# Optimization experiments

Hardware: AMD Instinct MI355X
Metric: run time of the kernel (lower is better)

The kernel has to match this reference:

```python
import jax, jax.numpy as jnp
import numpy as np

B, S, D, H, NUM_REL = 8, 1024, 1024, 16, 512
HD = D // H  # head size = 64


def setup_inputs() -> dict:
    key = jax.random.key(0)
    ks = jax.random.split(key, 12)
    sc = 0.02  # weight init scale for numerical stability
    inp = {
        "query": jax.random.normal(ks[0], (B, S, D), jnp.float32),
        "key": jax.random.normal(ks[1], (B, S, D), jnp.float32),
        "value": jax.random.normal(ks[2], (B, S, D), jnp.float32),
        "Wq": jax.random.normal(ks[3], (D, D), jnp.float32) * sc,
        "bq": jnp.zeros((D,), jnp.float32),
        "Wk": jax.random.normal(ks[4], (D, D), jnp.float32) * sc,
        "bk": jnp.zeros((D,), jnp.float32),
        "Wv": jax.random.normal(ks[5], (D, D), jnp.float32) * sc,
        "bv": jnp.zeros((D,), jnp.float32),
        "Wo": jax.random.normal(ks[6], (D, D), jnp.float32) * sc,
        "bo": jnp.zeros((D,), jnp.float32),
        "pos_table": jax.random.normal(ks[7], (NUM_REL, HD), jnp.float32) * sc,
        # True = masked position (causal: cannot attend to future)
        "mask": jnp.broadcast_to(jnp.triu(jnp.ones((S, S), bool), k=1), (B, S, S)),
    }
    return inp


def reference(query, key, value, Wq, bq, Wk, bk, Wv, bv, Wo, bo, pos_table, mask):
    Bq, Sq, Dm = query.shape
    hd = Dm // H

    def proj(x, W, b):
        # nn.Linear: x @ W.T + b, then split heads -> [B, H, S, hd]
        return (x @ W.T + b).reshape(Bq, Sq, H, hd).transpose(0, 2, 1, 3)

    q = proj(query, Wq, bq)
    k = proj(key, Wk, bk)
    v = proj(value, Wv, bv)

    scores = jnp.einsum("bhid,bhjd->bhij", q, k)

    # relative-position bias: idxs[i,j] = clip(i - j, 0, NUM_REL-1)
    t = jnp.arange(Sq)
    idxs = jnp.clip(t[:, None] - t[None, :], 0, pos_table.shape[0] - 1)
    pos = pos_table[idxs]  # [S, S, hd]
    scores = scores + jnp.einsum("bhid,ijd->bhij", q, pos)

    scores = scores / np.sqrt(hd).astype(np.float32)
    scores = jnp.where(mask[:, None, :, :], jnp.float32(-1e9), scores)
    prob = jax.nn.softmax(scores, axis=-1)  # dropout p=0.0 -> identity

    out = jnp.einsum("bhij,bhjd->bhid", prob, v)
    out = out.transpose(0, 2, 1, 3).reshape(Bq, Sq, Dm)
    return out @ Wo.T + bo
```

## Files before the change

### kernel.cpp

```cpp
#include <hip/hip_runtime.h>
#include <stdint.h>

#define DEV __device__ __forceinline__

typedef unsigned short u16;
typedef __bf16 bf16x8 __attribute__((ext_vector_type(8)));
typedef float  f32x4  __attribute__((ext_vector_type(4)));
typedef unsigned short u16x8 __attribute__((ext_vector_type(8)));
typedef unsigned short u16x4 __attribute__((ext_vector_type(4)));
typedef float  fvec4  __attribute__((ext_vector_type(4)));

constexpr int Sz   = 1024;
constexpr int Dm   = 1024;
constexpr int HDm  = 64;
constexpr int NREL = 512;
constexpr int Mrows = 8192;
constexpr int KV   = 32;

DEV u16 f2bf(float f) { return __builtin_bit_cast(u16, (__bf16)f); }
DEV float bf2f(u16 h) { return __builtin_bit_cast(float, (uint32_t)h << 16); }
DEV f32x4 mfma16(bf16x8 a, bf16x8 b, f32x4 c) {
  return __builtin_amdgcn_mfma_f32_16x16x32_bf16(a, b, c, 0, 0, 0);
}
DEV float ex2(float x) {
  float r;
  asm("v_exp_f32 %0, %1" : "=v"(r) : "v"(x));
  return r;
}

DEV u16x4 tr0(const u16* p) {
  u16x4 d;
  asm volatile("ds_read_b64_tr_b16 %0, %1"
               : "=v"(d)
               : "v"((const __attribute__((address_space(3))) u16*)p));
  return d;
}
DEV u16x4 tr512(const u16* p) {
  u16x4 d;
  asm volatile("ds_read_b64_tr_b16 %0, %1 offset:512"
               : "=v"(d)
               : "v"((const __attribute__((address_space(3))) u16*)p));
  return d;
}
DEV bf16x8 mk8(u16x4 a, u16x4 b) {
  u16x8 r;
  r[0] = a[0]; r[1] = a[1]; r[2] = a[2]; r[3] = a[3];
  r[4] = b[0]; r[5] = b[1]; r[6] = b[2]; r[7] = b[3];
  return __builtin_bit_cast(bf16x8, r);
}
DEV void gload(const u16* src, u16* dst) {
  __builtin_amdgcn_global_load_lds(
      (const __attribute__((address_space(1))) void*)src,
      (__attribute__((address_space(3))) void*)dst, 16, 0, 0);
}

__global__ __launch_bounds__(256) void cvtw_kernel(const float* __restrict__ w0,
                                                   const float* __restrict__ w1,
                                                   const float* __restrict__ w2,
                                                   const float* __restrict__ w3,
                                                   const float* __restrict__ ps,
                                                   u16* __restrict__ o0,
                                                   u16* __restrict__ o1,
                                                   u16* __restrict__ o2,
                                                   u16* __restrict__ o3,
                                                   u16* __restrict__ op) {
  const int bid = blockIdx.x;
  const float* in;
  u16* out;
  int local;
  if (bid < 4096) {
    const int s = bid >> 10;
    in = s == 0 ? w0 : s == 1 ? w1 : s == 2 ? w2 : w3;
    out = s == 0 ? o0 : s == 1 ? o1 : s == 2 ? o2 : o3;
    local = bid & 1023;
  } else {
    in = ps; out = op; local = bid - 4096;
  }
  size_t i = (size_t)local * 256 + threadIdx.x;
  fvec4 v = *(const fvec4*)(in + i * 4);
  u16x4 o;
  o[0] = f2bf(v[0]); o[1] = f2bf(v[1]); o[2] = f2bf(v[2]); o[3] = f2bf(v[3]);
  *(u16x4*)(out + i * 4) = o;
}

template<bool OUT_BF16>
DEV void gemm_epilogue(const float* bias, void* Cout, int m0, int n0,
                       int wr, int wc, int lr, int lg, f32x4 acc[4][4]) {
  #pragma unroll
  for (int m = 0; m < 4; ++m) {
    const int grow = m0 + wr + m * 16 + lr;
    #pragma unroll
    for (int n = 0; n < 4; ++n) {
      const int gcol = n0 + wc + n * 16 + lg * 4;
      fvec4 bb = *(const fvec4*)&bias[gcol];
      if (OUT_BF16) {
        u16x4 w;
        #pragma unroll
        for (int r = 0; r < 4; ++r) w[r] = f2bf(acc[m][n][r] + bb[r]);
        *(u16x4*)&((u16*)Cout)[(size_t)grow * Dm + gcol] = w;
      } else {
        fvec4 w;
        #pragma unroll
        for (int r = 0; r < 4; ++r) w[r] = acc[m][n][r] + bb[r];
        *(fvec4*)&((float*)Cout)[(size_t)grow * Dm + gcol] = w;
      }
    }
  }
}

DEV void gemm_compute(const u16* Ab, const u16* Bb, int wr, int wc,
                      int lr, int lg, f32x4 acc[4][4]) {
  #pragma unroll
  for (int kk = 0; kk < 2; ++kk) {
    bf16x8 af[4], bf_[4];
    #pragma unroll
    for (int m = 0; m < 4; ++m)
      af[m] = *(const bf16x8*)&Ab[(wr + m * 16 + lr) * 64 + (((kk * 4 + lg) ^ (lr & 7)) * 8)];
    #pragma unroll
    for (int n = 0; n < 4; ++n)
      bf_[n] = *(const bf16x8*)&Bb[(wc + n * 16 + lr) * 64 + (((kk * 4 + lg) ^ (lr & 7)) * 8)];
    __builtin_amdgcn_s_setprio(1);
    #pragma unroll
    for (int m = 0; m < 4; ++m)
      #pragma unroll
      for (int n = 0; n < 4; ++n)
        acc[m][n] = mfma16(bf_[n], af[m], acc[m][n]);
    __builtin_amdgcn_s_setprio(0);
  }
}

template<bool OUT_BF16>
DEV void gemm_body16(const u16* __restrict__ A, const u16* __restrict__ Bw,
                     const float* __restrict__ bias, void* __restrict__ Cout,
                     int m0, int n0, u16* As, u16* Bs) {
  const int tid = threadIdx.x;
  const int wave = tid >> 6, lane = tid & 63;
  const int lr = lane & 15, lg = lane >> 4;
  const int wr = (wave >> 1) * 64, wc = (wave & 1) * 64;

  auto issue = [&](int t) {
    const int k0 = t * 64;
    u16* Ad = As + (t & 1) * (128 * 64);
    u16* Bd = Bs + (t & 1) * (128 * 64);
    #pragma unroll
    for (int it = 0; it < 4; ++it) {
      int chunk = it * 256 + tid;
      int row = chunk >> 3, c16 = chunk & 7;
      gload(Bw + (size_t)(n0 + row) * Dm + k0 + ((c16 ^ (row & 7)) * 8),
            Bd + (it * 256 + wave * 64) * 8);
      gload(A + (size_t)(m0 + row) * Dm + k0 + ((c16 ^ (row & 7)) * 8),
            Ad + (it * 256 + wave * 64) * 8);
    }
  };

  issue(0);
  f32x4 acc[4][4] = {};
  for (int t = 0; t < 16; ++t) {
    if (t < 15) {
      issue(t + 1);
      asm volatile("s_waitcnt vmcnt(8)" ::: "memory");
    } else {
      asm volatile("s_waitcnt vmcnt(0)" ::: "memory");
    }
    __builtin_amdgcn_s_barrier();
    gemm_compute(As + (t & 1) * (128 * 64), Bs + (t & 1) * (128 * 64),
                 wr, wc, lr, lg, acc);
    __builtin_amdgcn_s_barrier();
  }
  gemm_epilogue<OUT_BF16>(bias, Cout, m0, n0, wr, wc, lr, lg, acc);
}

template<bool OUT_BF16>
DEV void gemm_body32(const float* __restrict__ A, const u16* __restrict__ Bw,
                     const float* __restrict__ bias, void* __restrict__ Cout,
                     int m0, int n0, u16* As, u16* Bs) {
  const int tid = threadIdx.x;
  const int wave = tid >> 6, lane = tid & 63;
  const int lr = lane & 15, lg = lane >> 4;
  const int wr = (wave >> 1) * 64, wc = (wave & 1) * 64;
  const int row = tid >> 3 << 2, c16 = tid & 7;

  auto issueB = [&](int t) {
    const int k0 = t * 64;
    u16* Bd = Bs + (t & 1) * (128 * 64);
    #pragma unroll
    for (int it = 0; it < 4; ++it) {
      int chunk = it * 256 + tid;
      int rw = chunk >> 3, cc = chunk & 7;
      gload(Bw + (size_t)(n0 + rw) * Dm + k0 + ((cc ^ (rw & 7)) * 8),
            Bd + (it * 256 + wave * 64) * 8);
    }
  };

  fvec4 ar[4][2];
  auto loadA = [&](int t) {
    const int k0 = t * 64;
    #pragma unroll
    for (int it = 0; it < 4; ++it) {
      int chunk = it * 256 + tid;
      int rw = chunk >> 3, cc = chunk & 7;
      const float* src = A + (size_t)(m0 + rw) * Dm + k0 + cc * 8;
      ar[it][0] = *(const fvec4*)src;
      ar[it][1] = *(const fvec4*)(src + 4);
    }
  };

  issueB(0);
  loadA(0);
  f32x4 acc[4][4] = {};
  for (int t = 0; t < 16; ++t) {
    asm volatile("s_waitcnt vmcnt(0)" ::: "memory");
    u16* Ad = As + (t & 1) * (128 * 64);
    #pragma unroll
    for (int it = 0; it < 4; ++it) {
      int chunk = it * 256 + tid;
      int rw = chunk >> 3, cc = chunk & 7;
      u16x8 v;
      #pragma unroll
      for (int e = 0; e < 4; ++e) { v[e] = f2bf(ar[it][0][e]); v[e + 4] = f2bf(ar[it][1][e]); }
      *(u16x8*)&Ad[rw * 64 + ((cc ^ (rw & 7)) * 8)] = v;
    }
    if (t < 15) { issueB(t + 1); loadA(t + 1); }
    asm volatile("s_waitcnt lgkmcnt(0)" ::: "memory");
    __builtin_amdgcn_s_barrier();
    gemm_compute(Ad, Bs + (t & 1) * (128 * 64), wr, wc, lr, lg, acc);
    __builtin_amdgcn_s_barrier();
  }
  gemm_epilogue<OUT_BF16>(bias, Cout, m0, n0, wr, wc, lr, lg, acc);
}

template<bool OUT_BF16>
__global__ __launch_bounds__(256) void gemm1_kernel(const u16* __restrict__ A,
                                                    const u16* __restrict__ Bw,
                                                    const float* __restrict__ bias,
                                                    void* __restrict__ Cout) {
  __shared__ u16 As[2 * 128 * 64];
  __shared__ u16 Bs[2 * 128 * 64];
  const int r = blockIdx.x;
  const int xcd = r & 7, loc = r >> 3;
  const int m0 = (xcd * 8 + (loc & 7)) * 128;
  const int n0 = (loc >> 3) * 128;
  gemm_body16<OUT_BF16>(A, Bw, bias, Cout, m0, n0, As, Bs);
}

__global__ __launch_bounds__(256) void gemm3_kernel(
    const float* __restrict__ Xq, const float* __restrict__ Xk, const float* __restrict__ Xv,
    const u16* __restrict__ Wq, const u16* __restrict__ Wk, const u16* __restrict__ Wv,
    const float* __restrict__ bq, const float* __restrict__ bk, const float* __restrict__ bv,
    u16* __restrict__ Cq, u16* __restrict__ Ck, u16* __restrict__ Cv) {
  __shared__ u16 As[2 * 128 * 64];
  __shared__ u16 Bs[2 * 128 * 64];
  const int flat = blockIdx.x;
  const int seg = flat >> 9;
  const int r = flat & 511;
  const int xcd = r & 7, loc = r >> 3;
  const int m0 = (xcd * 8 + (loc & 7)) * 128;
  const int n0 = (loc >> 3) * 128;
  const float* A = seg == 0 ? Xq : seg == 1 ? Xk : Xv;
  const u16* Bw = seg == 0 ? Wq : seg == 1 ? Wk : Wv;
  const float* bias = seg == 0 ? bq : seg == 1 ? bk : bv;
  u16* C = seg == 0 ? Cq : seg == 1 ? Ck : Cv;
  gemm_body32<true>(A, Bw, bias, C, m0, n0, As, Bs);
}

__global__ __launch_bounds__(256, 4) void attn_kernel(const u16* __restrict__ Q,
                                                      const u16* __restrict__ Kb,
                                                      const u16* __restrict__ Vb,
                                                      const u16* __restrict__ posB,
                                                      u16* __restrict__ O) {
  __shared__ u16 Ks[2][KV * 64];
  __shared__ u16 Vs[2][KV * 64];
  __shared__ u16 ring[128 * 64];
  __shared__ u16 SH[4][16 * 40];

  const int tid = threadIdx.x;
  const int wave = tid >> 6, lane = tid & 63;
  const int lr = lane & 15, lg = lane >> 4;
  const int bid = blockIdx.x;
  const int xcd = bid & 7;
  const int idx = bid >> 3;
  const int bhl = idx & 15;
  const int pp_ = idx >> 4;
  const int bh  = xcd * 16 + bhl;
  const int b = bh >> 4, h = bh & 15;

  u16* SHW = SH[wave];
  const size_t rowbase = (size_t)(b * Sz) * Dm + h * HDm;

  const int krow = tid >> 3, kc = tid & 7;
  const int vj = ((tid >> 5) << 2) | ((tid >> 1) & 3);
  const int vd = ((tid >> 3) & 3) * 16 + (tid & 1) * 8;
  const int rrow = tid >> 3, rcol = tid & 7;

  auto issueKV = [&](int t) {
    const int j0 = t * KV;
    const int bsel = t & 1;
    gload(Kb + rowbase + (size_t)(j0 + krow) * Dm + ((kc ^ (krow & 7)) * 8),
          &Ks[bsel][wave * 512]);
    gload(Vb + rowbase + (size_t)(j0 + vj) * Dm + vd, &Vs[bsel][wave * 512]);
  };
  auto stageRing = [&](int cb) {
    const int rel = cb + rrow;
    const int slot = rel & 127;
    const int cl = rel < 0 ? 0 : (rel > NREL - 1 ? NREL - 1 : rel);
    gload(posB + cl * 64 + ((rcol ^ (slot & 7)) * 8),
          &ring[((cb & 127) + wave * 8) * 64]);
  };

  constexpr float SC = 0.125f * 1.44269504f;

  for (int job = 0; job < 2; ++job) {
    const int qi = job ? pp_ : 15 - pp_;
    const int qb = qi * 64;
    const int wq = qb + wave * 16;
    const int nt = 2 * qi + 2;
    const int qg = wq + lr;

    const u16* qptr = Q + rowbase + (size_t)(wq + lr) * Dm;
    bf16x8 qf[2];
    qf[0] = *(const bf16x8*)(qptr + lg * 8);
    qf[1] = *(const bf16x8*)(qptr + 32 + lg * 8);

    float b511;
    {
      const u16* pp = posB + (NREL - 1) * HDm;
      bf16x8 pa0 = *(const bf16x8*)(pp + lg * 8);
      bf16x8 pa1 = *(const bf16x8*)(pp + 32 + lg * 8);
      f32x4 a = {};
      a = mfma16(pa0, qf[0], a);
      a = mfma16(pa1, qf[1], a);
      b511 = a[0];
    }

    stageRing(qb + 32);
    stageRing(qb);
    stageRing(qb - 32);
    issueKV(0);

    f32x4 oacc[4] = {};
    float m_i = -1e30f, l_i = 0.f;

    for (int t = 0; t < nt; ++t) {
      const int j0 = t * KV;
      const int bsel = t & 1;
      const bool active = (j0 <= wq + 15);
      const bool clamp = (wq - j0 - 31) >= NREL - 1;
      const int wb = wq - j0 - 31;

      if (t + 1 < nt) {
        stageRing(qb - 32 * (t + 1) - 32);
        issueKV(t + 1);
        asm volatile("s_waitcnt vmcnt(3)" ::: "memory");
      } else {
        asm volatile("s_waitcnt vmcnt(0)" ::: "memory");
      }
      __builtin_amdgcn_s_barrier();

      if (active) {
        if (!clamp) {
          #pragma unroll
          for (int wg = 0; wg < 3; ++wg) {
            const int rrel = wb + wg * 16 + lr;
            const int slot = rrel & 127;
            const u16* rp = &ring[slot * 64];
            f32x4 a = {};
            a = mfma16(qf[0], *(const bf16x8*)&rp[((0 + lg) ^ (slot & 7)) * 8], a);
            a = mfma16(qf[1], *(const bf16x8*)&rp[((4 + lg) ^ (slot & 7)) * 8], a);
            #pragma unroll
            for (int r = 0; r < 4; ++r) {
              const int q = lg * 4 + r;
              const int col = q - (wg * 16 + lr) + 31;
              if (col >= 0 && col < 32)
                SHW[q * 40 + col] = f2bf(a[r]);
            }
          }
        }

        __builtin_amdgcn_s_setprio(1);
        f32x4 s0 = {}, s1 = {};
        const u16* KT = &Ks[bsel][0];
        s0 = mfma16(*(const bf16x8*)&KT[(0 + lr) * 64 + (((0 + lg) ^ (lr & 7)) * 8)], qf[0], s0);
        s0 = mfma16(*(const bf16x8*)&KT[(0 + lr) * 64 + (((4 + lg) ^ (lr & 7)) * 8)], qf[1], s0);
        s1 = mfma16(*(const bf16x8*)&KT[(16 + lr) * 64 + (((0 + lg) ^ (lr & 7)) * 8)], qf[0], s1);
        s1 = mfma16(*(const bf16x8*)&KT[(16 + lr) * 64 + (((4 + lg) ^ (lr & 7)) * 8)], qf[1], s1);
        __builtin_amdgcn_s_setprio(0);

        float p0[4], p1[4];
        float tmax = -3e38f;
        if (clamp) {
          #pragma unroll
          for (int r = 0; r < 4; ++r) {
            p0[r] = (s0[r] + b511) * SC; tmax = fmaxf(tmax, p0[r]);
            p1[r] = (s1[r] + b511) * SC; tmax = fmaxf(tmax, p1[r]);
          }
        } else {
          u16x4 bv0 = *(const u16x4*)&SHW[lr * 40 + lg * 4];
          u16x4 bv1 = *(const u16x4*)&SHW[lr * 40 + 16 + lg * 4];
          #pragma unroll
          for (int r = 0; r < 4; ++r) {
            float v0 = (s0[r] + bf2f(bv0[r])) * SC;
            if (j0 + lg * 4 + r > qg) v0 = -1e9f;
            p0[r] = v0; tmax = fmaxf(tmax, v0);
            float v1 = (s1[r] + bf2f(bv1[r])) * SC;
            if (j0 + 16 + lg * 4 + r > qg) v1 = -1e9f;
            p1[r] = v1; tmax = fmaxf(tmax, v1);
          }
        }
        tmax = fmaxf(tmax, __shfl_xor(tmax, 16));
        tmax = fmaxf(tmax, __shfl_xor(tmax, 32));

        if (!__all(tmax <= m_i + 11.5f)) {
          float mn = fmaxf(m_i, tmax);
          float sc = ex2(m_i - mn);
          m_i = mn; l_i *= sc;
          #pragma unroll
          for (int dg = 0; dg < 4; ++dg) oacc[dg] *= sc;
        }

        float lsum = 0.f;
        #pragma unroll
        for (int r = 0; r < 4; ++r) {
          p0[r] = ex2(p0[r] - m_i); lsum += p0[r];
          p1[r] = ex2(p1[r] - m_i); lsum += p1[r];
        }
        lsum += __shfl_xor(lsum, 16);
        lsum += __shfl_xor(lsum, 32);
        l_i += lsum;

        u16x4 pk0, pk1;
        #pragma unroll
        for (int r = 0; r < 4; ++r) { pk0[r] = f2bf(p0[r]); pk1[r] = f2bf(p1[r]); }
        *(u16x4*)&SHW[lr * 40 + lg * 4] = pk0;
        *(u16x4*)&SHW[lr * 40 + 16 + lg * 4] = pk1;

        bf16x8 pB = *(const bf16x8*)&SHW[lr * 40 + lg * 8];

        u16x4 va[4][2];
        #pragma unroll
        for (int dg = 0; dg < 4; ++dg) {
          const u16* base = &Vs[bsel][(2 * lg) * 256 + dg * 64 + lr * 4];
          va[dg][0] = tr0(base);
          va[dg][1] = tr512(base);
        }
        asm volatile("s_waitcnt lgkmcnt(0)" ::: "memory");
        __builtin_amdgcn_sched_barrier(0);
        __builtin_amdgcn_s_setprio(1);
        #pragma unroll
        for (int dg = 0; dg < 4; ++dg)
          oacc[dg] = mfma16(mk8(va[dg][0], va[dg][1]), pB, oacc[dg]);
        __builtin_amdgcn_s_setprio(0);
      }
      __builtin_amdgcn_s_barrier();
    }

    const float inv = 1.0f / l_i;
    const size_t obase = rowbase + (size_t)qg * Dm;
    #pragma unroll
    for (int dg = 0; dg < 4; ++dg) {
      u16x4 w;
      #pragma unroll
      for (int r = 0; r < 4; ++r) w[r] = f2bf(oacc[dg][r] * inv);
      *(u16x4*)&O[obase + dg * 16 + lg * 4] = w;
    }
  }
}

extern "C" void kernel_launch(void* const* d_in, const int* in_sizes, int n_in,
                              void* d_out, int out_size, void* d_ws, size_t ws_size,
                              hipStream_t stream) {
  const float* query = (const float*)d_in[0];
  const float* key   = (const float*)d_in[1];
  const float* value = (const float*)d_in[2];
  const float* Wq    = (const float*)d_in[3];
  const float* bq    = (const float*)d_in[4];
  const float* Wk    = (const float*)d_in[5];
  const float* bk    = (const float*)d_in[6];
  const float* Wv    = (const float*)d_in[7];
  const float* bv    = (const float*)d_in[8];
  const float* Wo    = (const float*)d_in[9];
  const float* bo    = (const float*)d_in[10];
  const float* pos   = (const float*)d_in[11];

  char* ws = (char*)d_ws;
  u16* WqB  = (u16*)(ws);
  u16* WkB  = (u16*)(ws + (2ull << 20));
  u16* WvB  = (u16*)(ws + (4ull << 20));
  u16* WoB  = (u16*)(ws + (6ull << 20));
  u16* posB = (u16*)(ws + (8ull << 20));
  u16* Qb   = (u16*)(ws + (9ull << 20));
  u16* Kb   = (u16*)(ws + (25ull << 20));
  u16* Vb   = (u16*)(ws + (41ull << 20));
  u16* Ob   = (u16*)(ws + (57ull << 20));

  cvtw_kernel<<<4128, 256, 0, stream>>>(Wq, Wk, Wv, Wo, pos,
                                        WqB, WkB, WvB, WoB, posB);

  gemm3_kernel<<<1536, 256, 0, stream>>>(query, key, value, WqB, WkB, WvB,
                                         bq, bk, bv, Qb, Kb, Vb);

  attn_kernel<<<1024, 256, 0, stream>>>(Qb, Kb, Vb, posB, Ob);

  gemm1_kernel<false><<<512, 256, 0, stream>>>(Ob, WoB, bo, d_out);
}
```

Baseline: 185.0 us.

## Shrink GEMM K-tile to 32 with triple-buffered LDS and deeper prefetch

Both projection GEMM bodies move from a 64-wide K tile with double buffering to a 32-wide K tile with three rotating LDS buffers and a prefetch distance of two tiles. The A operand in the fp32 GEMM is held in two alternating register sets and written into a single bf16 LDS tile. The swizzle changes to fit 32-element rows, and launch bounds now request 4 blocks per CU. This cuts LDS use per block to raise occupancy and hide global-load latency, at the cost of twice as many barriers per K and more register pressure.

```diff
diff --git a/kernel.cpp b/kernel.cpp
--- a/kernel.cpp
+++ b/kernel.cpp
@@ -108,25 +108,28 @@
   }
 }
 
-DEV void gemm_compute(const u16* Ab, const u16* Bb, int wr, int wc,
-                      int lr, int lg, f32x4 acc[4][4]) {
+DEV void gemm_compute32(const u16* Ab, const u16* Bb, int wr, int wc,
+                        int lr, int lg, f32x4 (&acc)[4][4]) {
+  bf16x8 af[4], bf_[4];
   #pragma unroll
-  for (int kk = 0; kk < 2; ++kk) {
-    bf16x8 af[4], bf_[4];
-    #pragma unroll
-    for (int m = 0; m < 4; ++m)
-      af[m] = *(const bf16x8*)&Ab[(wr + m * 16 + lr) * 64 + (((kk * 4 + lg) ^ (lr & 7)) * 8)];
+  for (int m = 0; m < 4; ++m) {
+    const int row = wr + m * 16 + lr;
+    const int s = ((row >> 2) ^ row) & 3;
+    af[m] = *(const bf16x8*)&Ab[row * 32 + ((lg ^ s) * 8)];
+  }
+  #pragma unroll
+  for (int n = 0; n < 4; ++n) {
+    const int row = wc + n * 16 + lr;
+    const int s = ((row >> 2) ^ row) & 3;
+    bf_[n] = *(const bf16x8*)&Bb[row * 32 + ((lg ^ s) * 8)];
+  }
+  __builtin_amdgcn_s_setprio(1);
+  #pragma unroll
+  for (int m = 0; m < 4; ++m)
     #pragma unroll
     for (int n = 0; n < 4; ++n)
-      bf_[n] = *(const bf16x8*)&Bb[(wc + n * 16 + lr) * 64 + (((kk * 4 + lg) ^ (lr & 7)) * 8)];
-    __builtin_amdgcn_s_setprio(1);
-    #pragma unroll
-    for (int m = 0; m < 4; ++m)
-      #pragma unroll
-      for (int n = 0; n < 4; ++n)
-        acc[m][n] = mfma16(bf_[n], af[m], acc[m][n]);
-    __builtin_amdgcn_s_setprio(0);
-  }
+      acc[m][n] = mfma16(bf_[n], af[m], acc[m][n]);
+  __builtin_amdgcn_s_setprio(0);
 }
 
 template<bool OUT_BF16>
@@ -139,32 +142,34 @@
   const int wr = (wave >> 1) * 64, wc = (wave & 1) * 64;
 
   auto issue = [&](int t) {
-    const int k0 = t * 64;
-    u16* Ad = As + (t & 1) * (128 * 64);
-    u16* Bd = Bs + (t & 1) * (128 * 64);
+    const int k0 = t * 32;
+    u16* Ad = As + (t % 3) * (128 * 32);
+    u16* Bd = Bs + (t % 3) * (128 * 32);
     #pragma unroll
-    for (int it = 0; it < 4; ++it) {
-      int chunk = it * 256 + tid;
-      int row = chunk >> 3, c16 = chunk & 7;
-      gload(Bw + (size_t)(n0 + row) * Dm + k0 + ((c16 ^ (row & 7)) * 8),
-            Bd + (it * 256 + wave * 64) * 8);
-      gload(A + (size_t)(m0 + row) * Dm + k0 + ((c16 ^ (row & 7)) * 8),
-            Ad + (it * 256 + wave * 64) * 8);
+    for (int c = 0; c < 2; ++c) {
+      const int chunk = c * 256 + tid;
+      const int row = chunk >> 2, g = chunk & 3;
+      const int s = ((row >> 2) ^ row) & 3;
+      gload(A + (size_t)(m0 + row) * Dm + k0 + ((g ^ s) * 8),
+            Ad + c * 2048 + wave * 512);
+      gload(Bw + (size_t)(n0 + row) * Dm + k0 + ((g ^ s) * 8),
+            Bd + c * 2048 + wave * 512);
     }
   };
 
   issue(0);
+  issue(1);
   f32x4 acc[4][4] = {};
-  for (int t = 0; t < 16; ++t) {
-    if (t < 15) {
-      issue(t + 1);
-      asm volatile("s_waitcnt vmcnt(8)" ::: "memory");
+  for (int t = 0; t < 32; ++t) {
+    if (t < 31) {
+      asm volatile("s_waitcnt vmcnt(4)" ::: "memory");
     } else {
       asm volatile("s_waitcnt vmcnt(0)" ::: "memory");
     }
+    if (t < 30) issue(t + 2);
     __builtin_amdgcn_s_barrier();
-    gemm_compute(As + (t & 1) * (128 * 64), Bs + (t & 1) * (128 * 64),
-                 wr, wc, lr, lg, acc);
+    gemm_compute32(As + (t % 3) * (128 * 32), Bs + (t % 3) * (128 * 32),
+                   wr, wc, lr, lg, acc);
     __builtin_amdgcn_s_barrier();
   }
   gemm_epilogue<OUT_BF16>(bias, Cout, m0, n0, wr, wc, lr, lg, acc);
@@ -178,64 +183,72 @@
   const int wave = tid >> 6, lane = tid & 63;
   const int lr = lane & 15, lg = lane >> 4;
   const int wr = (wave >> 1) * 64, wc = (wave & 1) * 64;
-  const int row = tid >> 3 << 2, c16 = tid & 7;
-
+  const int arow = tid >> 1, ach = tid & 1;
+  const int as_ = ((arow >> 2) ^ arow) & 3;
+
+  auto loadA = [&](int t, fvec4 (&arr)[4]) {
+    const float* src = A + (size_t)(m0 + arow) * Dm + t * 32 + ach * 16;
+    arr[0] = *(const fvec4*)src;
+    arr[1] = *(const fvec4*)(src + 4);
+    arr[2] = *(const fvec4*)(src + 8);
+    arr[3] = *(const fvec4*)(src + 12);
+  };
   auto issueB = [&](int t) {
-    const int k0 = t * 64;
-    u16* Bd = Bs + (t & 1) * (128 * 64);
+    u16* Bd = Bs + (t % 3) * (128 * 32);
     #pragma unroll
-    for (int it = 0; it < 4; ++it) {
-      int chunk = it * 256 + tid;
-      int rw = chunk >> 3, cc = chunk & 7;
-      gload(Bw + (size_t)(n0 + rw) * Dm + k0 + ((cc ^ (rw & 7)) * 8),
-            Bd + (it * 256 + wave * 64) * 8);
-    }
-  };
-
-  fvec4 ar[4][2];
-  auto loadA = [&](int t) {
-    const int k0 = t * 64;
+    for (int c = 0; c < 2; ++c) {
+      const int chunk = c * 256 + tid;
+      const int row = chunk >> 2, g = chunk & 3;
+      const int s = ((row >> 2) ^ row) & 3;
+      gload(Bw + (size_t)(n0 + row) * Dm + t * 32 + ((g ^ s) * 8),
+            Bd + c * 2048 + wave * 512);
+    }
+  };
+  auto writeA = [&](fvec4 (&arr)[4]) {
+    u16x8 w0, w1;
     #pragma unroll
-    for (int it = 0; it < 4; ++it) {
-      int chunk = it * 256 + tid;
-      int rw = chunk >> 3, cc = chunk & 7;
-      const float* src = A + (size_t)(m0 + rw) * Dm + k0 + cc * 8;
-      ar[it][0] = *(const fvec4*)src;
-      ar[it][1] = *(const fvec4*)(src + 4);
-    }
-  };
-
+    for (int e = 0; e < 4; ++e) {
+      w0[e] = f2bf(arr[0][e]); w0[e + 4] = f2bf(arr[1][e]);
+      w1[e] = f2bf(arr[2][e]); w1[e + 4] = f2bf(arr[3][e]);
+    }
+    *(u16x8*)&As[arow * 32 + (((2 * ach + 0) ^ as_) * 8)] = w0;
+    *(u16x8*)&As[arow * 32 + (((2 * ach + 1) ^ as_) * 8)] = w1;
+  };
+
+  fvec4 ar0[4], ar1[4];
+  loadA(0, ar0);
   issueB(0);
-  loadA(0);
+  loadA(1, ar1);
+  issueB(1);
+
   f32x4 acc[4][4] = {};
-  for (int t = 0; t < 16; ++t) {
-    asm volatile("s_waitcnt vmcnt(0)" ::: "memory");
-    u16* Ad = As + (t & 1) * (128 * 64);
-    #pragma unroll
-    for (int it = 0; it < 4; ++it) {
-      int chunk = it * 256 + tid;
-      int rw = chunk >> 3, cc = chunk & 7;
-      u16x8 v;
-      #pragma unroll
-      for (int e = 0; e < 4; ++e) { v[e] = f2bf(ar[it][0][e]); v[e + 4] = f2bf(ar[it][1][e]); }
-      *(u16x8*)&Ad[rw * 64 + ((cc ^ (rw & 7)) * 8)] = v;
-    }
-    if (t < 15) { issueB(t + 1); loadA(t + 1); }
+  auto step = [&](int t, fvec4 (&arr)[4]) {
+    if (t < 31) {
+      asm volatile("s_waitcnt vmcnt(6)" ::: "memory");
+    } else {
+      asm volatile("s_waitcnt vmcnt(0)" ::: "memory");
+    }
+    writeA(arr);
+    if (t < 30) { loadA(t + 2, arr); issueB(t + 2); }
     asm volatile("s_waitcnt lgkmcnt(0)" ::: "memory");
     __builtin_amdgcn_s_barrier();
-    gemm_compute(Ad, Bs + (t & 1) * (128 * 64), wr, wc, lr, lg, acc);
+    gemm_compute32(As, Bs + (t % 3) * (128 * 32), wr, wc, lr, lg, acc);
     __builtin_amdgcn_s_barrier();
+  };
+  for (int t = 0; t < 32; t += 2) {
+    step(t, ar0);
+    step(t + 1, ar1);
   }
   gemm_epilogue<OUT_BF16>(bias, Cout, m0, n0, wr, wc, lr, lg, acc);
 }
 
 template<bool OUT_BF16>
-__global__ __launch_bounds__(256) void gemm1_kernel(const u16* __restrict__ A,
-                                                    const u16* __restrict__ Bw,
-                                                    const float* __restrict__ bias,
-                                                    void* __restrict__ Cout) {
-  __shared__ u16 As[2 * 128 * 64];
-  __shared__ u16 Bs[2 * 128 * 64];
+__global__ __launch_bounds__(256, 4) void gemm1_kernel(const u16* __restrict__ A,
+                                                       const u16* __restrict__ Bw,
+                                                       const float* __restrict__ bias,
+                                                       void* __restrict__ Cout) {
+  __shared__ u16 As[3 * 128 * 32];
+  __shared__ u16 Bs[3 * 128 * 32];
   const int r = blockIdx.x;
   const int xcd = r & 7, loc = r >> 3;
   const int m0 = (xcd * 8 + (loc & 7)) * 128;
@@ -243,13 +256,13 @@
   gemm_body16<OUT_BF16>(A, Bw, bias, Cout, m0, n0, As, Bs);
 }
 
-__global__ __launch_bounds__(256) void gemm3_kernel(
+__global__ __launch_bounds__(256, 4) void gemm3_kernel(
     const float* __restrict__ Xq, const float* __restrict__ Xk, const float* __restrict__ Xv,
     const u16* __restrict__ Wq, const u16* __restrict__ Wk, const u16* __restrict__ Wv,
     const float* __restrict__ bq, const float* __restrict__ bk, const float* __restrict__ bv,
     u16* __restrict__ Cq, u16* __restrict__ Ck, u16* __restrict__ Cv) {
-  __shared__ u16 As[2 * 128 * 64];
-  __shared__ u16 Bs[2 * 128 * 64];
+  __shared__ u16 As[128 * 32];
+  __shared__ u16 Bs[3 * 128 * 32];
   const int flat = blockIdx.x;
   const int seg = flat >> 9;
   const int r = flat & 511;
```

Measured after the change: 320.5 us. 73.3% more time.
